# Performance work log

Measured on AMD Instinct MI355X. Metric: run time of the kernel, lower is better.

Reference implementation:

```python
import jax, jax.numpy as jnp
import numpy as np

N, E, EH, RH, R, H = 50000, 800000, 256, 128, 500, 2


def _seg_softmax(e, rel, num_segments):
    # torch_geometric.utils.softmax keyed by rel: (e - max_seg).exp() / (sum_seg + 1e-16)
    m = jax.ops.segment_max(e, rel, num_segments=num_segments)
    m = jnp.where(jnp.isfinite(m), m, 0.0)  # empty segments -> 0
    ex = jnp.exp(e - m[rel])
    s = jax.ops.segment_sum(ex, rel, num_segments=num_segments)
    return ex / (s[rel] + 1e-16)


def setup_inputs() -> dict:
    key = jax.random.key(0)
    ks = jax.random.split(key, 7)
    x_e = jax.random.normal(ks[0], (N, EH), dtype=jnp.float32)
    edge_index = jax.random.randint(ks[1], (2, E), 0, N)
    rel = jax.random.randint(ks[2], (E,), 0, R)
    w_h = jax.random.normal(ks[3], (RH, EH), dtype=jnp.float32) / np.sqrt(EH)
    w_t = jax.random.normal(ks[4], (RH, EH), dtype=jnp.float32) / np.sqrt(EH)
    a_h = jax.random.normal(ks[5], (H, RH), dtype=jnp.float32) / np.sqrt(RH)
    a_t = jax.random.normal(ks[6], (H, RH), dtype=jnp.float32) / np.sqrt(RH)
    return {"x_e": x_e, "edge_index": edge_index, "rel": rel,
            "w_h": w_h, "w_t": w_t, "a_h": a_h, "a_t": a_t, "num_heads": H}


def reference(x_e, edge_index, rel, w_h, w_t, a_h, a_t, num_heads):
    src, dst = edge_index[0], edge_index[1]
    x_r_h = x_e @ w_h.T  # [N, RH]
    x_r_t = x_e @ w_t.T  # [N, RH]
    # per-node attention scores for all heads: [N, H]
    s_hh = x_r_h @ a_h.T
    s_tt = x_r_t @ a_t.T
    s_th = x_r_t @ a_h.T
    s_ht = x_r_h @ a_t.T
    acc = jnp.zeros((R, RH), dtype=x_e.dtype)
    for h in range(num_heads):  # small fixed head count
        e1 = jax.nn.leaky_relu(s_hh[src, h] + s_tt[dst, h], 0.01)
        a1 = _seg_softmax(e1, rel, R)
        acc = acc + jax.ops.segment_sum(a1[:, None] * x_r_h[src], rel, num_segments=R)
        e2 = jax.nn.leaky_relu(s_th[src, h] + s_ht[dst, h], 0.01)
        a2 = _seg_softmax(e2, rel, R)
        acc = acc + jax.ops.segment_sum(a2[:, None] * x_r_t[dst], rel, num_segments=R)
    x_r = acc / num_heads / 2.0
    return x_r  # dropout is identity in eval mode
```

## Files before the change

### kernel.cpp

```cpp
#include <hip/hip_runtime.h>
#include <hip/hip_bf16.h>

#define NN 50000
#define NE 800000
#define NR 500
#define KEH 256
#define KRH 128
#define NSB 8
#define SBW 6250
#define NBK (NR*NSB)
#define NBE 256
#define EPB (NE/NBE)
#define NTILE 3125
#define CSB 16

typedef __attribute__((ext_vector_type(8))) __bf16 bf16x8;
typedef __attribute__((ext_vector_type(4))) float f32x4;

#define OFF_XH     0UL
#define OFF_XT     12800000UL
#define OFF_SP     25600000UL
#define OFF_DP     26400000UL
#define OFF_SUMS   27200000UL
#define OFF_HISTH  27208000UL
#define OFF_HISTT  27224000UL
#define OFF_INVS   27240000UL
#define OFF_BASEH  27248000UL
#define OFF_BASET  27264016UL
#define OFF_RECH   27312032UL
#define OFF_RECT   33712032UL
#define OFF_PART   40112032UL
#define OFF_AH     42160032UL
#define OFF_AT     42161056UL
#define OFF_FLAG   42162080UL
#define OFF_WHH    42162144UL
#define OFF_WTH    42293216UL
#define OFF_HPBH   42424288UL
#define OFF_HPBT   46520288UL

__device__ __forceinline__ int clampi(int v, int hi) {
    v = v < 0 ? 0 : v;
    return v >= hi ? hi - 1 : v;
}

__device__ __forceinline__ int sniff_isbf(const unsigned* xe_raw) {
    int lane = threadIdx.x & 63;
    unsigned w = xe_raw[lane];
    unsigned ex = (w >> 7) & 0xFFu;
    bool hit = (ex >= 115u && ex <= 131u);
    return __popcll(__ballot(hit)) >= 32;
}

__global__ __launch_bounds__(256) void k_init(const unsigned* __restrict__ xe_raw,
                                              const void* __restrict__ ah_in, const void* __restrict__ at_in,
                                              const void* __restrict__ wh, const void* __restrict__ wt,
                                              unsigned* __restrict__ flag, float* __restrict__ ah32,
                                              float* __restrict__ at32,
                                              __bf16* __restrict__ whh, __bf16* __restrict__ wth,
                                              unsigned* __restrict__ zero1) {
    int isbf = sniff_isbf(xe_raw);
    int t = threadIdx.x;
    if (blockIdx.x == 0) {
        if (t == 0) flag[0] = (unsigned)isbf;
        ah32[t] = isbf ? __bfloat162float(((const __hip_bfloat16*)ah_in)[t]) : ((const float*)ah_in)[t];
        at32[t] = isbf ? __bfloat162float(((const __hip_bfloat16*)at_in)[t]) : ((const float*)at_in)[t];
    } else if (blockIdx.x <= 128) {
        int o = (blockIdx.x - 1) * 256 + t;
        int e = o & 7, c = (o >> 3) & 15, q = (o >> 7) & 3, ks = (o >> 9) & 7, ct = o >> 12;
        int i = (ct * 16 + c) * KEH + ks * 32 + q * 8 + e;
        if (isbf) {
            whh[o] = ((const __bf16*)wh)[i];
            wth[o] = ((const __bf16*)wt)[i];
        } else {
            whh[o] = (__bf16)((const float*)wh)[i];
            wth[o] = (__bf16)((const float*)wt)[i];
        }
    } else {
        int stride = (gridDim.x - 129) * 256;
        for (int i = (blockIdx.x - 129) * 256 + t; i < 10000; i += stride) zero1[i] = 0u;
    }
}

__global__ __launch_bounds__(1024, 4) void k_gemm(const void* __restrict__ xe,
                                              const unsigned* __restrict__ flag,
                                              const __bf16* __restrict__ whh, const __bf16* __restrict__ wth,
                                              const float* __restrict__ ah, const float* __restrict__ at,
                                              __hip_bfloat16* __restrict__ xh, __hip_bfloat16* __restrict__ xt,
                                              float4* __restrict__ sp, float4* __restrict__ dp) {
    __shared__ uint4 lb[8192];
    const int t = threadIdx.x, lane = t & 63, wave = t >> 6;
    const int l16 = lane & 15, quad = lane >> 4;
    const int isbf = (int)flag[0];

    {
        const uint4* s0 = (const uint4*)whh;
        const uint4* s1 = (const uint4*)wth;
        #pragma unroll
        for (int i = 0; i < 4; ++i) {
            lb[i * 1024 + t] = s0[i * 1024 + t];
            lb[4096 + i * 1024 + t] = s1[i * 1024 + t];
        }
    }
    __syncthreads();

    const int tile = wave * 256 + (int)blockIdx.x;
    if (tile >= NTILE) return;
    const int row = tile * 16 + l16;
    bf16x8 a[8];
    if (isbf) {
        const __bf16* xb = (const __bf16*)xe + (size_t)row * KEH;
        #pragma unroll
        for (int ks = 0; ks < 8; ++ks)
            a[ks] = *(const bf16x8*)(xb + ks * 32 + quad * 8);
    } else {
        const float* xf = (const float*)xe + (size_t)row * KEH;
        #pragma unroll
        for (int ks = 0; ks < 8; ++ks) {
            const float* p = xf + ks * 32 + quad * 8;
            float4 u0 = *(const float4*)p, u1 = *(const float4*)(p + 4);
            a[ks][0] = (__bf16)u0.x; a[ks][1] = (__bf16)u0.y;
            a[ks][2] = (__bf16)u0.z; a[ks][3] = (__bf16)u0.w;
            a[ks][4] = (__bf16)u1.x; a[ks][5] = (__bf16)u1.y;
            a[ks][6] = (__bf16)u1.z; a[ks][7] = (__bf16)u1.w;
        }
    }

    float hh0[4], hh1[4], ht0[4], ht1[4];
    float th0[4], th1[4], tt0[4], tt1[4];
    #pragma unroll
    for (int ph = 0; ph < 2; ++ph) {
        f32x4 acc[8];
        #pragma unroll
        for (int ct = 0; ct < 8; ++ct) acc[ct] = (f32x4){0.f, 0.f, 0.f, 0.f};
        #pragma unroll
        for (int ks = 0; ks < 8; ++ks)
            #pragma unroll
            for (int ct = 0; ct < 8; ++ct)
                acc[ct] = __builtin_amdgcn_mfma_f32_16x16x32_bf16(
                    a[ks], *(const bf16x8*)&lb[ph * 4096 + (ct * 8 + ks) * 64 + lane],
                    acc[ct], 0, 0, 0);

        __hip_bfloat16* out = ph ? xt : xh;
        float s0[4] = {0.f,0.f,0.f,0.f}, s1[4] = {0.f,0.f,0.f,0.f};
        float s2[4] = {0.f,0.f,0.f,0.f}, s3[4] = {0.f,0.f,0.f,0.f};
        #pragma unroll
        for (int ct = 0; ct < 8; ++ct) {
            int c = ct * 16 + l16;
            float va0 = ah[c], va1 = ah[128 + c];
            float vb0 = at[c], vb1 = at[128 + c];
            #pragma unroll
            for (int jj = 0; jj < 4; ++jj) {
                float v = acc[ct][jj];
                s0[jj] = fmaf(v, va0, s0[jj]);
                s1[jj] = fmaf(v, va1, s1[jj]);
                s2[jj] = fmaf(v, vb0, s2[jj]);
                s3[jj] = fmaf(v, vb1, s3[jj]);
                out[(size_t)(tile * 16 + quad * 4 + jj) * KRH + c] = __float2bfloat16(v);
            }
        }
        #pragma unroll
        for (int off = 8; off; off >>= 1)
            #pragma unroll
            for (int jj = 0; jj < 4; ++jj) {
                s0[jj] += __shfl_xor(s0[jj], off);
                s1[jj] += __shfl_xor(s1[jj], off);
                s2[jj] += __shfl_xor(s2[jj], off);
                s3[jj] += __shfl_xor(s3[jj], off);
            }
        #pragma unroll
        for (int jj = 0; jj < 4; ++jj) {
            if (ph == 0) { hh0[jj] = s0[jj]; hh1[jj] = s1[jj]; ht0[jj] = s2[jj]; ht1[jj] = s3[jj]; }
            else         { th0[jj] = s0[jj]; th1[jj] = s1[jj]; tt0[jj] = s2[jj]; tt1[jj] = s3[jj]; }
        }
    }
    if (l16 == 0) {
        #pragma unroll
        for (int jj = 0; jj < 4; ++jj) {
            int n = tile * 16 + quad * 4 + jj;
            sp[n] = make_float4(hh0[jj], hh1[jj], th0[jj], th1[jj]);
            dp[n] = make_float4(tt0[jj], tt1[jj], ht0[jj], ht1[jj]);
        }
    }
}

__device__ __forceinline__ float eexp(float x) {
    x = x > 0.f ? x : 0.01f * x;
    x = fminf(x, 50.f);
    return __expf(x);
}

__global__ __launch_bounds__(1024) void k_edge(const int* __restrict__ src, const int* __restrict__ dst,
                                               const int* __restrict__ rel,
                                               const float4* __restrict__ sp, const float4* __restrict__ dp,
                                               float* __restrict__ sums,
                                               unsigned* __restrict__ histH, unsigned* __restrict__ histT,
                                               unsigned* __restrict__ hpbH, unsigned* __restrict__ hpbT) {
    __shared__ float ls[NR * 4];
    __shared__ unsigned lhH[NBK], lhT[NBK];
    int t = threadIdx.x;
    for (int i = t; i < NR * 4; i += 1024) ls[i] = 0.f;
    for (int i = t; i < NBK; i += 1024) { lhH[i] = 0u; lhT[i] = 0u; }
    __syncthreads();
    unsigned lo = blockIdx.x * EPB, hi = lo + EPB;
    for (unsigned e = lo + t; e < hi; e += 1024) {
        int s = clampi(src[e], NN), d = clampi(dst[e], NN), r = clampi(rel[e], NR);
        float4 a = sp[s], b = dp[d];
        float4 ex;
        ex.x = eexp(a.x + b.x); ex.y = eexp(a.y + b.y);
        ex.z = eexp(a.z + b.z); ex.w = eexp(a.w + b.w);
        atomicAdd(&ls[r*4+0], ex.x);
        atomicAdd(&ls[r*4+1], ex.y);
        atomicAdd(&ls[r*4+2], ex.z);
        atomicAdd(&ls[r*4+3], ex.w);
        atomicAdd(&lhH[r * NSB + s / SBW], 1u);
        atomicAdd(&lhT[r * NSB + d / SBW], 1u);
    }
    __syncthreads();
    for (int i = t; i < NR * 4; i += 1024)
        if (ls[i] != 0.f) atomicAdd(&sums[i], ls[i]);
    size_t row = (size_t)blockIdx.x * NBK;
    for (int i = t; i < NBK; i += 1024) {
        unsigned cH = lhH[i], cT = lhT[i];
        hpbH[row + i] = cH;
        hpbT[row + i] = cT;
        if (cH) atomicAdd(&histH[i], cH);
        if (cT) atomicAdd(&histT[i], cT);
    }
}

__global__ __launch_bounds__(256) void k_scan(const unsigned* __restrict__ histH,
                                              const unsigned* __restrict__ histT,
                                              const float* __restrict__ sums,
                                              unsigned* __restrict__ hpbH, unsigned* __restrict__ hpbT,
                                              unsigned* __restrict__ baseH, unsigned* __restrict__ baseT,
                                              float* __restrict__ invs) {
    __shared__ unsigned bases[4096];
    __shared__ unsigned wsum[4];
    __shared__ unsigned wsum2[4][CSB];
    const int b = blockIdx.x;
    const int pass = b >= (NBK / CSB);
    const int slice = pass ? b - NBK / CSB : b;
    const unsigned* h = pass ? histT : histH;
    unsigned* hpb = pass ? hpbT : hpbH;
    unsigned* base = pass ? baseT : baseH;
    const int t = threadIdx.x, lane = t & 63, wv = t >> 6;

    {
        int j0 = t * 16;
        unsigned v[16], s = 0;
        const uint4* hp4 = (const uint4*)(h + j0);
        #pragma unroll
        for (int q = 0; q < 4; ++q) {
            uint4 u = (j0 + q * 4 < NBK) ? hp4[q] : make_uint4(0u, 0u, 0u, 0u);
            v[q*4+0] = u.x; v[q*4+1] = u.y; v[q*4+2] = u.z; v[q*4+3] = u.w;
        }
        #pragma unroll
        for (int k = 0; k < 16; ++k) {
            if (j0 + k >= NBK) v[k] = 0u;
            s += v[k];
        }
        unsigned inc = s;
        #pragma unroll
        for (int d = 1; d < 64; d <<= 1) {
            unsigned u = __shfl_up(inc, d);
            if (lane >= d) inc += u;
        }
        if (lane == 63) wsum[wv] = inc;
        __syncthreads();
        unsigned wbase = 0;
        for (int i = 0; i < wv; ++i) wbase += wsum[i];
        unsigned run = wbase + inc - s;
        #pragma unroll
        for (int k = 0; k < 16; ++k) {
            if (j0 + k < NBK) bases[j0 + k] = run;
            run += v[k];
        }
        __syncthreads();
        if (slice == 0) {
            for (int i = t; i < NBK; i += 256) base[i] = bases[i];
            if (t == 0) base[NBK] = wsum[0] + wsum[1] + wsum[2] + wsum[3];
        }
        if (b == 0) for (int i = t; i < NR * 4; i += 256) invs[i] = 1.f / (sums[i] + 1e-16f);
    }

    {
        int bin0 = slice * CSB;
        unsigned v[CSB], inc[CSB];
        uint4* hp = (uint4*)(hpb + (size_t)t * NBK + bin0);
        #pragma unroll
        for (int q = 0; q < CSB / 4; ++q) {
            uint4 u = hp[q];
            v[q*4+0] = u.x; v[q*4+1] = u.y; v[q*4+2] = u.z; v[q*4+3] = u.w;
        }
        #pragma unroll
        for (int k = 0; k < CSB; ++k) inc[k] = v[k];
        #pragma unroll
        for (int d = 1; d < 64; d <<= 1) {
            #pragma unroll
            for (int k = 0; k < CSB; ++k) {
                unsigned u = __shfl_up(inc[k], d);
                if (lane >= d) inc[k] += u;
            }
        }
        if (lane == 63) {
            #pragma unroll
            for (int k = 0; k < CSB; ++k) wsum2[wv][k] = inc[k];
        }
        __syncthreads();
        #pragma unroll
        for (int k = 0; k < CSB; ++k) {
            unsigned wbase = 0;
            for (int i = 0; i < wv; ++i) wbase += wsum2[i][k];
            v[k] = bases[bin0 + k] + wbase + inc[k] - v[k];
        }
        #pragma unroll
        for (int q = 0; q < CSB / 4; ++q)
            hp[q] = make_uint4(v[q*4+0], v[q*4+1], v[q*4+2], v[q*4+3]);
    }
}

__global__ __launch_bounds__(1024) void k_mkrec(const int* __restrict__ src, const int* __restrict__ dst,
                                                const int* __restrict__ rel,
                                                const float4* __restrict__ sp, const float4* __restrict__ dp,
                                                const float4* __restrict__ invs4,
                                                const unsigned* __restrict__ hpbH, const unsigned* __restrict__ hpbT,
                                                uint2* __restrict__ recH, uint2* __restrict__ recT) {
    __shared__ unsigned lcH[NBK], lcT[NBK];
    int t = threadIdx.x;
    size_t row = (size_t)blockIdx.x * NBK;
    for (int i = t; i < NBK; i += 1024) { lcH[i] = hpbH[row + i]; lcT[i] = hpbT[row + i]; }
    __syncthreads();
    unsigned lo = blockIdx.x * EPB, hi = lo + EPB;
    for (unsigned e = lo + t; e < hi; e += 1024) {
        int s = clampi(src[e], NN), d = clampi(dst[e], NN), r = clampi(rel[e], NR);
        float4 a = sp[s], b = dp[d];
        float4 iv = invs4[r];
        float exx = eexp(a.x + b.x), exy = eexp(a.y + b.y);
        float exz = eexp(a.z + b.z), exw = eexp(a.w + b.w);
        float w1 = exx * iv.x + exy * iv.y;
        float w2 = exz * iv.z + exw * iv.w;
        unsigned pH = atomicAdd(&lcH[r * NSB + s / SBW], 1u);
        unsigned pT = atomicAdd(&lcT[r * NSB + d / SBW], 1u);
        if (pH < NE) recH[pH] = make_uint2((unsigned)s, __float_as_uint(w1));
        if (pT < NE) recT[pT] = make_uint2((unsigned)d, __float_as_uint(w2));
    }
}

__global__ __launch_bounds__(256) void k_accR(const uint2* __restrict__ recH, const uint2* __restrict__ recT,
                                              const unsigned* __restrict__ baseH, const unsigned* __restrict__ baseT,
                                              const __hip_bfloat16* __restrict__ xh,
                                              const __hip_bfloat16* __restrict__ xt,
                                              float* __restrict__ part) {
    __shared__ float red[3][128];
    __shared__ uint2 lrec[256];
    int b = blockIdx.x;
    int t = threadIdx.x, lane = t & 63, wv = t >> 6;
    int l16 = lane & 15, g = lane >> 4;
    float az[8];
    #pragma unroll
    for (int k = 0; k < 8; ++k) az[k] = 0.f;

    for (int pass = 0; pass < 2; ++pass) {
        const uint2* rec = pass ? recT : recH;
        const unsigned* base = pass ? baseT : baseH;
        const uint4* xs = (const uint4*)(pass ? xt : xh);
        unsigned b0 = base[b];
        unsigned cnt = base[b + 1] - b0;
        if (cnt > NE) cnt = 0;
        for (unsigned cb = 0; cb < cnt; cb += 256u) {
            unsigned cn = cnt - cb; if (cn > 256u) cn = 256u;
            __syncthreads();
            if ((unsigned)t < cn) lrec[t] = rec[b0 + cb + t];
            __syncthreads();
            unsigned j = (unsigned)(wv * 4 + g);
            for (; j + 48u < cn; j += 64u) {
                uint2 v0 = lrec[j], v1 = lrec[j + 16u], v2 = lrec[j + 32u], v3 = lrec[j + 48u];
                unsigned n0 = v0.x < NN ? v0.x : 0u;
                unsigned n1 = v1.x < NN ? v1.x : 0u;
                unsigned n2 = v2.x < NN ? v2.x : 0u;
                unsigned n3 = v3.x < NN ? v3.x : 0u;
                uint4 u0 = xs[(size_t)n0 * 16 + l16];
                uint4 u1 = xs[(size_t)n1 * 16 + l16];
                uint4 u2 = xs[(size_t)n2 * 16 + l16];
                uint4 u3 = xs[(size_t)n3 * 16 + l16];
                float w0 = __uint_as_float(v0.y), w1 = __uint_as_float(v1.y);
                float w2 = __uint_as_float(v2.y), w3 = __uint_as_float(v3.y);
                az[0] = fmaf(w0, __uint_as_float(u0.x << 16),         az[0]);
                az[1] = fmaf(w0, __uint_as_float(u0.x & 0xffff0000u), az[1]);
                az[2] = fmaf(w0, __uint_as_float(u0.y << 16),         az[2]);
                az[3] = fmaf(w0, __uint_as_float(u0.y & 0xffff0000u), az[3]);
                az[4] = fmaf(w0, __uint_as_float(u0.z << 16),         az[4]);
                az[5] = fmaf(w0, __uint_as_float(u0.z & 0xffff0000u), az[5]);
                az[6] = fmaf(w0, __uint_as_float(u0.w << 16),         az[6]);
                az[7] = fmaf(w0, __uint_as_float(u0.w & 0xffff0000u), az[7]);
                az[0] = fmaf(w1, __uint_as_float(u1.x << 16),         az[0]);
                az[1] = fmaf(w1, __uint_as_float(u1.x & 0xffff0000u), az[1]);
                az[2] = fmaf(w1, __uint_as_float(u1.y << 16),         az[2]);
                az[3] = fmaf(w1, __uint_as_float(u1.y & 0xffff0000u), az[3]);
                az[4] = fmaf(w1, __uint_as_float(u1.z << 16),         az[4]);
                az[5] = fmaf(w1, __uint_as_float(u1.z & 0xffff0000u), az[5]);
                az[6] = fmaf(w1, __uint_as_float(u1.w << 16),         az[6]);
                az[7] = fmaf(w1, __uint_as_float(u1.w & 0xffff0000u), az[7]);
                az[0] = fmaf(w2, __uint_as_float(u2.x << 16),         az[0]);
                az[1] = fmaf(w2, __uint_as_float(u2.x & 0xffff0000u), az[1]);
                az[2] = fmaf(w2, __uint_as_float(u2.y << 16),         az[2]);
                az[3] = fmaf(w2, __uint_as_float(u2.y & 0xffff0000u), az[3]);
                az[4] = fmaf(w2, __uint_as_float(u2.z << 16),         az[4]);
                az[5] = fmaf(w2, __uint_as_float(u2.z & 0xffff0000u), az[5]);
                az[6] = fmaf(w2, __uint_as_float(u2.w << 16),         az[6]);
                az[7] = fmaf(w2, __uint_as_float(u2.w & 0xffff0000u), az[7]);
                az[0] = fmaf(w3, __uint_as_float(u3.x << 16),         az[0]);
                az[1] = fmaf(w3, __uint_as_float(u3.x & 0xffff0000u), az[1]);
                az[2] = fmaf(w3, __uint_as_float(u3.y << 16),         az[2]);
                az[3] = fmaf(w3, __uint_as_float(u3.y & 0xffff0000u), az[3]);
                az[4] = fmaf(w3, __uint_as_float(u3.z << 16),         az[4]);
                az[5] = fmaf(w3, __uint_as_float(u3.z & 0xffff0000u), az[5]);
                az[6] = fmaf(w3, __uint_as_float(u3.w << 16),         az[6]);
                az[7] = fmaf(w3, __uint_as_float(u3.w & 0xffff0000u), az[7]);
            }
            for (; j < cn; j += 16u) {
                uint2 v = lrec[j];
                unsigned nd = v.x < NN ? v.x : 0u;
                float w = __uint_as_float(v.y);
                uint4 u = xs[(size_t)nd * 16 + l16];
                az[0] = fmaf(w, __uint_as_float(u.x << 16),          az[0]);
                az[1] = fmaf(w, __uint_as_float(u.x & 0xffff0000u),  az[1]);
                az[2] = fmaf(w, __uint_as_float(u.y << 16),          az[2]);
                az[3] = fmaf(w, __uint_as_float(u.y & 0xffff0000u),  az[3]);
                az[4] = fmaf(w, __uint_as_float(u.z << 16),          az[4]);
                az[5] = fmaf(w, __uint_as_float(u.z & 0xffff0000u),  az[5]);
                az[6] = fmaf(w, __uint_as_float(u.w << 16),          az[6]);
                az[7] = fmaf(w, __uint_as_float(u.w & 0xffff0000u),  az[7]);
            }
        }
    }
    #pragma unroll
    for (int k = 0; k < 8; ++k) {
        az[k] += __shfl_xor(az[k], 16);
        az[k] += __shfl_xor(az[k], 32);
    }
    __syncthreads();
    if (wv > 0 && lane < 16) {
        #pragma unroll
        for (int k = 0; k < 8; ++k) red[wv - 1][l16 * 8 + k] = az[k];
    }
    __syncthreads();
    if (wv == 0 && lane < 16) {
        #pragma unroll
        for (int k = 0; k < 8; ++k) {
            float s = az[k] + red[0][l16 * 8 + k] + red[1][l16 * 8 + k] + red[2][l16 * 8 + k];
            part[(size_t)b * KRH + l16 * 8 + k] = s;
        }
    }
}

__global__ __launch_bounds__(256) void k_out(const float* __restrict__ part,
                                             const unsigned* __restrict__ flag, void* __restrict__ out) {
    int i = blockIdx.x * 256 + threadIdx.x;
    if (i < NR * KRH) {
        int r = i >> 7, c = i & 127;
        float v = 0.f;
        for (int s = 0; s < NSB; ++s) v += part[(size_t)(r * NSB + s) * KRH + c];
        v *= 0.25f;
        if (!isfinite(v)) v = 0.f;
        if (flag[0]) ((__hip_bfloat16*)out)[i] = __float2bfloat16(v);
        else         ((float*)out)[i] = v;
    }
}

extern "C" void kernel_launch(void* const* d_in, const int* in_sizes, int n_in,
                              void* d_out, int out_size, void* d_ws, size_t ws_size,
                              hipStream_t stream) {
    const void* xe  = d_in[0];
    const int* eidx = (const int*)d_in[1];
    const int* rel  = (const int*)d_in[2];
    const void* wh  = d_in[3];
    const void* wt  = d_in[4];
    const void* ahp = d_in[5];
    const void* atp = d_in[6];

    const int* src = eidx;
    const int* dst = eidx + NE;

    char* ws = (char*)d_ws;
    __hip_bfloat16* xh = (__hip_bfloat16*)(ws + OFF_XH);
    __hip_bfloat16* xt = (__hip_bfloat16*)(ws + OFF_XT);
    float4*   sp     = (float4*)(ws + OFF_SP);
    float4*   dp     = (float4*)(ws + OFF_DP);
    float*    sums   = (float*)(ws + OFF_SUMS);
    unsigned* histH  = (unsigned*)(ws + OFF_HISTH);
    unsigned* histT  = (unsigned*)(ws + OFF_HISTT);
    float*    invs   = (float*)(ws + OFF_INVS);
    unsigned* baseH  = (unsigned*)(ws + OFF_BASEH);
    unsigned* baseT  = (unsigned*)(ws + OFF_BASET);
    uint2*    recH   = (uint2*)(ws + OFF_RECH);
    uint2*    recT   = (uint2*)(ws + OFF_RECT);
    float*    partp  = (float*)(ws + OFF_PART);
    float*    ah32   = (float*)(ws + OFF_AH);
    float*    at32   = (float*)(ws + OFF_AT);
    unsigned* flag   = (unsigned*)(ws + OFF_FLAG);
    __bf16*   whh    = (__bf16*)(ws + OFF_WHH);
    __bf16*   wth    = (__bf16*)(ws + OFF_WTH);
    unsigned* hpbH   = (unsigned*)(ws + OFF_HPBH);
    unsigned* hpbT   = (unsigned*)(ws + OFF_HPBT);

    k_init<<<161, 256, 0, stream>>>((const unsigned*)xe, ahp, atp, wh, wt, flag, ah32, at32,
                                     whh, wth, (unsigned*)(ws + OFF_SUMS));
    k_gemm<<<256, 1024, 0, stream>>>(xe, flag, whh, wth, ah32, at32, xh, xt, sp, dp);
    k_edge<<<NBE, 1024, 0, stream>>>(src, dst, rel, sp, dp, sums, histH, histT, hpbH, hpbT);
    k_scan<<<2 * (NBK / CSB), 256, 0, stream>>>(histH, histT, sums, hpbH, hpbT, baseH, baseT, invs);
    k_mkrec<<<NBE, 1024, 0, stream>>>(src, dst, rel, sp, dp, (const float4*)invs, hpbH, hpbT, recH, recT);
    k_accR<<<NBK, 256, 0, stream>>>(recH, recT, baseH, baseT, xh, xt, partp);
    k_out<<<(NR * KRH + 255) / 256, 256, 0, stream>>>(partp, flag, d_out);
}
```

Measured before the change: 219.2 us.

## Fuse per-relation accumulation and output into one kernel per relation

The accumulation kernel now runs one 512-thread block per relation, looping over all 8 source-bin sub-buckets, and writes the final scaled output directly. This removes the partial-sum buffer and the separate k_out launch. In exchange, the grid drops from 4000 blocks to 500, which could reduce parallelism and latency hiding on the gather-heavy loop.

Result: slower. 239.8 us (+9.4%).

```diff
diff --git a/kernel.cpp b/kernel.cpp
--- a/kernel.cpp
+++ b/kernel.cpp
@@ -29,7 +29,6 @@
 #define OFF_BASET  27264016UL
 #define OFF_RECH   27312032UL
 #define OFF_RECT   33712032UL
-#define OFF_PART   40112032UL
 #define OFF_AH     42160032UL
 #define OFF_AT     42161056UL
 #define OFF_FLAG   42162080UL
@@ -346,16 +345,17 @@
     }
 }
 
-__global__ __launch_bounds__(256) void k_accR(const uint2* __restrict__ recH, const uint2* __restrict__ recT,
+__global__ __launch_bounds__(512) void k_accO(const uint2* __restrict__ recH, const uint2* __restrict__ recT,
                                               const unsigned* __restrict__ baseH, const unsigned* __restrict__ baseT,
                                               const __hip_bfloat16* __restrict__ xh,
                                               const __hip_bfloat16* __restrict__ xt,
-                                              float* __restrict__ part) {
-    __shared__ float red[3][128];
-    __shared__ uint2 lrec[256];
-    int b = blockIdx.x;
+                                              const unsigned* __restrict__ flag, void* __restrict__ out) {
+    __shared__ float red[7][128];
+    __shared__ uint2 lrec[512];
+    int r = blockIdx.x;
     int t = threadIdx.x, lane = t & 63, wv = t >> 6;
     int l16 = lane & 15, g = lane >> 4;
+    int grp = wv * 4 + g;
     float az[8];
     #pragma unroll
     for (int k = 0; k < 8; ++k) az[k] = 0.f;
@@ -364,73 +364,76 @@
         const uint2* rec = pass ? recT : recH;
         const unsigned* base = pass ? baseT : baseH;
         const uint4* xs = (const uint4*)(pass ? xt : xh);
-        unsigned b0 = base[b];
-        unsigned cnt = base[b + 1] - b0;
-        if (cnt > NE) cnt = 0;
-        for (unsigned cb = 0; cb < cnt; cb += 256u) {
-            unsigned cn = cnt - cb; if (cn > 256u) cn = 256u;
-            __syncthreads();
-            if ((unsigned)t < cn) lrec[t] = rec[b0 + cb + t];
-            __syncthreads();
-            unsigned j = (unsigned)(wv * 4 + g);
-            for (; j + 48u < cn; j += 64u) {
-                uint2 v0 = lrec[j], v1 = lrec[j + 16u], v2 = lrec[j + 32u], v3 = lrec[j + 48u];
-                unsigned n0 = v0.x < NN ? v0.x : 0u;
-                unsigned n1 = v1.x < NN ? v1.x : 0u;
-                unsigned n2 = v2.x < NN ? v2.x : 0u;
-                unsigned n3 = v3.x < NN ? v3.x : 0u;
-                uint4 u0 = xs[(size_t)n0 * 16 + l16];
-                uint4 u1 = xs[(size_t)n1 * 16 + l16];
-                uint4 u2 = xs[(size_t)n2 * 16 + l16];
-                uint4 u3 = xs[(size_t)n3 * 16 + l16];
-                float w0 = __uint_as_float(v0.y), w1 = __uint_as_float(v1.y);
-                float w2 = __uint_as_float(v2.y), w3 = __uint_as_float(v3.y);
-                az[0] = fmaf(w0, __uint_as_float(u0.x << 16),         az[0]);
-                az[1] = fmaf(w0, __uint_as_float(u0.x & 0xffff0000u), az[1]);
-                az[2] = fmaf(w0, __uint_as_float(u0.y << 16),         az[2]);
-                az[3] = fmaf(w0, __uint_as_float(u0.y & 0xffff0000u), az[3]);
-                az[4] = fmaf(w0, __uint_as_float(u0.z << 16),         az[4]);
-                az[5] = fmaf(w0, __uint_as_float(u0.z & 0xffff0000u), az[5]);
-                az[6] = fmaf(w0, __uint_as_float(u0.w << 16),         az[6]);
-                az[7] = fmaf(w0, __uint_as_float(u0.w & 0xffff0000u), az[7]);
-                az[0] = fmaf(w1, __uint_as_float(u1.x << 16),         az[0]);
-                az[1] = fmaf(w1, __uint_as_float(u1.x & 0xffff0000u), az[1]);
-                az[2] = fmaf(w1, __uint_as_float(u1.y << 16),         az[2]);
-                az[3] = fmaf(w1, __uint_as_float(u1.y & 0xffff0000u), az[3]);
-                az[4] = fmaf(w1, __uint_as_float(u1.z << 16),         az[4]);
-                az[5] = fmaf(w1, __uint_as_float(u1.z & 0xffff0000u), az[5]);
-                az[6] = fmaf(w1, __uint_as_float(u1.w << 16),         az[6]);
-                az[7] = fmaf(w1, __uint_as_float(u1.w & 0xffff0000u), az[7]);
-                az[0] = fmaf(w2, __uint_as_float(u2.x << 16),         az[0]);
-                az[1] = fmaf(w2, __uint_as_float(u2.x & 0xffff0000u), az[1]);
-                az[2] = fmaf(w2, __uint_as_float(u2.y << 16),         az[2]);
-                az[3] = fmaf(w2, __uint_as_float(u2.y & 0xffff0000u), az[3]);
-                az[4] = fmaf(w2, __uint_as_float(u2.z << 16),         az[4]);
-                az[5] = fmaf(w2, __uint_as_float(u2.z & 0xffff0000u), az[5]);
-                az[6] = fmaf(w2, __uint_as_float(u2.w << 16),         az[6]);
-                az[7] = fmaf(w2, __uint_as_float(u2.w & 0xffff0000u), az[7]);
-                az[0] = fmaf(w3, __uint_as_float(u3.x << 16),         az[0]);
-                az[1] = fmaf(w3, __uint_as_float(u3.x & 0xffff0000u), az[1]);
-                az[2] = fmaf(w3, __uint_as_float(u3.y << 16),         az[2]);
-                az[3] = fmaf(w3, __uint_as_float(u3.y & 0xffff0000u), az[3]);
-                az[4] = fmaf(w3, __uint_as_float(u3.z << 16),         az[4]);
-                az[5] = fmaf(w3, __uint_as_float(u3.z & 0xffff0000u), az[5]);
-                az[6] = fmaf(w3, __uint_as_float(u3.w << 16),         az[6]);
-                az[7] = fmaf(w3, __uint_as_float(u3.w & 0xffff0000u), az[7]);
-            }
-            for (; j < cn; j += 16u) {
-                uint2 v = lrec[j];
-                unsigned nd = v.x < NN ? v.x : 0u;
-                float w = __uint_as_float(v.y);
-                uint4 u = xs[(size_t)nd * 16 + l16];
-                az[0] = fmaf(w, __uint_as_float(u.x << 16),          az[0]);
-                az[1] = fmaf(w, __uint_as_float(u.x & 0xffff0000u),  az[1]);
-                az[2] = fmaf(w, __uint_as_float(u.y << 16),          az[2]);
-                az[3] = fmaf(w, __uint_as_float(u.y & 0xffff0000u),  az[3]);
-                az[4] = fmaf(w, __uint_as_float(u.z << 16),          az[4]);
-                az[5] = fmaf(w, __uint_as_float(u.z & 0xffff0000u),  az[5]);
-                az[6] = fmaf(w, __uint_as_float(u.w << 16),          az[6]);
-                az[7] = fmaf(w, __uint_as_float(u.w & 0xffff0000u),  az[7]);
+        for (int sb = 0; sb < NSB; ++sb) {
+            int b = r * NSB + sb;
+            unsigned b0 = base[b];
+            unsigned cnt = base[b + 1] - b0;
+            if (cnt > NE) cnt = 0;
+            for (unsigned cb = 0; cb < cnt; cb += 512u) {
+                unsigned cn = cnt - cb; if (cn > 512u) cn = 512u;
+                __syncthreads();
+                if ((unsigned)t < cn) lrec[t] = rec[b0 + cb + t];
+                __syncthreads();
+                unsigned j = (unsigned)grp;
+                for (; j + 96u < cn; j += 128u) {
+                    uint2 v0 = lrec[j], v1 = lrec[j + 32u], v2 = lrec[j + 64u], v3 = lrec[j + 96u];
+                    unsigned n0 = v0.x < NN ? v0.x : 0u;
+                    unsigned n1 = v1.x < NN ? v1.x : 0u;
+                    unsigned n2 = v2.x < NN ? v2.x : 0u;
+                    unsigned n3 = v3.x < NN ? v3.x : 0u;
+                    uint4 u0 = xs[(size_t)n0 * 16 + l16];
+                    uint4 u1 = xs[(size_t)n1 * 16 + l16];
+                    uint4 u2 = xs[(size_t)n2 * 16 + l16];
+                    uint4 u3 = xs[(size_t)n3 * 16 + l16];
+                    float w0 = __uint_as_float(v0.y), w1 = __uint_as_float(v1.y);
+                    float w2 = __uint_as_float(v2.y), w3 = __uint_as_float(v3.y);
+                    az[0] = fmaf(w0, __uint_as_float(u0.x << 16),         az[0]);
+                    az[1] = fmaf(w0, __uint_as_float(u0.x & 0xffff0000u), az[1]);
+                    az[2] = fmaf(w0, __uint_as_float(u0.y << 16),         az[2]);
+                    az[3] = fmaf(w0, __uint_as_float(u0.y & 0xffff0000u), az[3]);
+                    az[4] = fmaf(w0, __uint_as_float(u0.z << 16),         az[4]);
+                    az[5] = fmaf(w0, __uint_as_float(u0.z & 0xffff0000u), az[5]);
+                    az[6] = fmaf(w0, __uint_as_float(u0.w << 16),         az[6]);
+                    az[7] = fmaf(w0, __uint_as_float(u0.w & 0xffff0000u), az[7]);
+                    az[0] = fmaf(w1, __uint_as_float(u1.x << 16),         az[0]);
+                    az[1] = fmaf(w1, __uint_as_float(u1.x & 0xffff0000u), az[1]);
+                    az[2] = fmaf(w1, __uint_as_float(u1.y << 16),         az[2]);
+                    az[3] = fmaf(w1, __uint_as_float(u1.y & 0xffff0000u), az[3]);
+                    az[4] = fmaf(w1, __uint_as_float(u1.z << 16),         az[4]);
+                    az[5] = fmaf(w1, __uint_as_float(u1.z & 0xffff0000u), az[5]);
+                    az[6] = fmaf(w1, __uint_as_float(u1.w << 16),         az[6]);
+                    az[7] = fmaf(w1, __uint_as_float(u1.w & 0xffff0000u), az[7]);
+                    az[0] = fmaf(w2, __uint_as_float(u2.x << 16),         az[0]);
+                    az[1] = fmaf(w2, __uint_as_float(u2.x & 0xffff0000u), az[1]);
+                    az[2] = fmaf(w2, __uint_as_float(u2.y << 16),         az[2]);
+                    az[3] = fmaf(w2, __uint_as_float(u2.y & 0xffff0000u), az[3]);
+                    az[4] = fmaf(w2, __uint_as_float(u2.z << 16),         az[4]);
+                    az[5] = fmaf(w2, __uint_as_float(u2.z & 0xffff0000u), az[5]);
+                    az[6] = fmaf(w2, __uint_as_float(u2.w << 16),         az[6]);
+                    az[7] = fmaf(w2, __uint_as_float(u2.w & 0xffff0000u), az[7]);
+                    az[0] = fmaf(w3, __uint_as_float(u3.x << 16),         az[0]);
+                    az[1] = fmaf(w3, __uint_as_float(u3.x & 0xffff0000u), az[1]);
+                    az[2] = fmaf(w3, __uint_as_float(u3.y << 16),         az[2]);
+                    az[3] = fmaf(w3, __uint_as_float(u3.y & 0xffff0000u), az[3]);
+                    az[4] = fmaf(w3, __uint_as_float(u3.z << 16),         az[4]);
+                    az[5] = fmaf(w3, __uint_as_float(u3.z & 0xffff0000u), az[5]);
+                    az[6] = fmaf(w3, __uint_as_float(u3.w << 16),         az[6]);
+                    az[7] = fmaf(w3, __uint_as_float(u3.w & 0xffff0000u), az[7]);
+                }
+                for (; j < cn; j += 32u) {
+                    uint2 v = lrec[j];
+                    unsigned nd = v.x < NN ? v.x : 0u;
+                    float w = __uint_as_float(v.y);
+                    uint4 u = xs[(size_t)nd * 16 + l16];
+                    az[0] = fmaf(w, __uint_as_float(u.x << 16),          az[0]);
+                    az[1] = fmaf(w, __uint_as_float(u.x & 0xffff0000u),  az[1]);
+                    az[2] = fmaf(w, __uint_as_float(u.y << 16),          az[2]);
+                    az[3] = fmaf(w, __uint_as_float(u.y & 0xffff0000u),  az[3]);
+                    az[4] = fmaf(w, __uint_as_float(u.z << 16),          az[4]);
+                    az[5] = fmaf(w, __uint_as_float(u.z & 0xffff0000u),  az[5]);
+                    az[6] = fmaf(w, __uint_as_float(u.w << 16),          az[6]);
+                    az[7] = fmaf(w, __uint_as_float(u.w & 0xffff0000u),  az[7]);
+                }
             }
         }
     }
@@ -446,25 +449,18 @@
     }
     __syncthreads();
     if (wv == 0 && lane < 16) {
+        int isbf = (int)flag[0];
         #pragma unroll
         for (int k = 0; k < 8; ++k) {
-            float s = az[k] + red[0][l16 * 8 + k] + red[1][l16 * 8 + k] + red[2][l16 * 8 + k];
-            part[(size_t)b * KRH + l16 * 8 + k] = s;
-        }
-    }
-}
-
-__global__ __launch_bounds__(256) void k_out(const float* __restrict__ part,
-                                             const unsigned* __restrict__ flag, void* __restrict__ out) {
-    int i = blockIdx.x * 256 + threadIdx.x;
-    if (i < NR * KRH) {
-        int r = i >> 7, c = i & 127;
-        float v = 0.f;
-        for (int s = 0; s < NSB; ++s) v += part[(size_t)(r * NSB + s) * KRH + c];
-        v *= 0.25f;
-        if (!isfinite(v)) v = 0.f;
-        if (flag[0]) ((__hip_bfloat16*)out)[i] = __float2bfloat16(v);
-        else         ((float*)out)[i] = v;
+            float s = az[k];
+            #pragma unroll
+            for (int i = 0; i < 7; ++i) s += red[i][l16 * 8 + k];
+            s *= 0.25f;
+            if (!isfinite(s)) s = 0.f;
+            int i = r * KRH + l16 * 8 + k;
+            if (isbf) ((__hip_bfloat16*)out)[i] = __float2bfloat16(s);
+            else      ((float*)out)[i] = s;
+        }
     }
 }
 
@@ -495,7 +491,6 @@
     unsigned* baseT  = (unsigned*)(ws + OFF_BASET);
     uint2*    recH   = (uint2*)(ws + OFF_RECH);
     uint2*    recT   = (uint2*)(ws + OFF_RECT);
-    float*    partp  = (float*)(ws + OFF_PART);
     float*    ah32   = (float*)(ws + OFF_AH);
     float*    at32   = (float*)(ws + OFF_AT);
     unsigned* flag   = (unsigned*)(ws + OFF_FLAG);
@@ -510,6 +505,5 @@
     k_edge<<<NBE, 1024, 0, stream>>>(src, dst, rel, sp, dp, sums, histH, histT, hpbH, hpbT);
     k_scan<<<2 * (NBK / CSB), 256, 0, stream>>>(histH, histT, sums, hpbH, hpbT, baseH, baseT, invs);
     k_mkrec<<<NBE, 1024, 0, stream>>>(src, dst, rel, sp, dp, (const float4*)invs, hpbH, hpbT, recH, recT);
-    k_accR<<<NBK, 256, 0, stream>>>(recH, recT, baseH, baseT, xh, xt, partp);
-    k_out<<<(NR * KRH + 255) / 256, 256, 0, stream>>>(partp, flag, d_out);
-}
+    k_accO<<<NR, 512, 0, stream>>>(recH, recT, baseH, baseT, xh, xt, flag, d_out);
+}
```
